# Optimization experiments

Hardware: AMD Instinct MI355X
Metric: run time of the kernel (lower is better)

Reference implementation:

```python
import jax, jax.numpy as jnp
import numpy as np

B, L, DIM, H = 2, 2048, 2048, 16
DH = DIM // H  # 128, size_per_head


def setup_inputs() -> dict:
    key = jax.random.key(0)
    k1, k2, k3, k4, k5, k6 = jax.random.split(key, 6)
    s = 0.02
    return {
        "query_tensor": jax.random.normal(k1, (B, L, DIM), jnp.float32),
        "value_tensor": jax.random.normal(k2, (B, L, DIM), jnp.float32),
        "attention_mask": jax.random.randint(k3, (B, L), 0, 2).astype(jnp.float32),
        "Wq": jax.random.normal(k4, (DIM, DIM), jnp.float32) * s,
        "Wk": jax.random.normal(k5, (DIM, DIM), jnp.float32) * s,
        "Wv": jax.random.normal(k6, (DIM, DIM), jnp.float32) * s,
    }


def reference(query_tensor, value_tensor, attention_mask, Wq, Wk, Wv):
    b, lq, dim = query_tensor.shape
    lv = value_tensor.shape[1]
    # torch Linear: x @ W.T (no bias)
    q = query_tensor @ Wq.T   # [B, Lq, DIM]
    k = value_tensor @ Wk.T   # [B, Lv, DIM]
    v = value_tensor @ Wv.T   # [B, Lv, DIM]
    # split heads -> [B, H, L, DH]
    q = q.reshape(b, lq, H, DH).transpose(0, 2, 1, 3)
    k = k.reshape(b, lv, H, DH).transpose(0, 2, 1, 3)
    v = v.reshape(b, lv, H, DH).transpose(0, 2, 1, 3)
    scores = jnp.einsum('bhqd,bhkd->bhqk', q, k) / jnp.sqrt(jnp.float32(DH))
    # multiplicative per-query mask, broadcast [B,1,Lq,1] -> [B,H,Lq,Lv]
    scores = scores * attention_mask[:, None, :, None]
    probs = jax.nn.softmax(scores, axis=-1)
    attn = jnp.einsum('bhqk,bhkd->bhqd', probs, v)  # [B,H,Lq,DH]
    return attn.transpose(0, 2, 1, 3).reshape(b, lq, dim)
```

## Files before the change

### kernel.cpp

```cpp
#include <hip/hip_runtime.h>
#include <hip/hip_bf16.h>
#include <stdint.h>

#define DIM_ 2048
#define L_   2048
#define B_   2
#define H_   16
#define DH_  128
#define NT_  32

#define QSCALE_ 0.12751743f

typedef __attribute__((ext_vector_type(4))) float fp32x4;
typedef __attribute__((ext_vector_type(8))) short s16x8;

__device__ __forceinline__ unsigned short bf16_rne(float f) {
    unsigned u = __builtin_bit_cast(unsigned, f);
    u += 0x7fffu + ((u >> 16) & 1u);
    return (unsigned short)(u >> 16);
}

__device__ __forceinline__ fp32x4 MFMA(s16x8 a, s16x8 b, fp32x4 c) {
    return __builtin_amdgcn_mfma_f32_16x16x32_bf16(a, b, c, 0, 0, 0);
}

__device__ __forceinline__ void gld16(const void* g, void* l) {
    auto gp = reinterpret_cast<const uint32_t __attribute__((address_space(1)))*>(
        reinterpret_cast<uintptr_t>(g));
    auto lp = reinterpret_cast<uint32_t __attribute__((address_space(3)))*>(
        reinterpret_cast<uintptr_t>(l));
    __builtin_amdgcn_global_load_lds(gp, lp, 16, 0, 0);
}

__device__ __forceinline__ float exp2_raw(float x) {
    float r; asm("v_exp_f32 %0, %1" : "=v"(r) : "v"(x)); return r;
}

__device__ __forceinline__ unsigned cvtpk_bf16(float a, float b) {
    unsigned r; asm("v_cvt_pk_bf16_f32 %0, %1, %2" : "=v"(r) : "v"(a), "v"(b)); return r;
}

__global__ void __launch_bounds__(256)
cvt_all(const float* __restrict__ query, const float* __restrict__ value,
        const float* __restrict__ Wq, const float* __restrict__ Wk,
        const float* __restrict__ Wv,
        unsigned short* __restrict__ qb, unsigned short* __restrict__ vb,
        unsigned short* __restrict__ wqb, unsigned short* __restrict__ wkb,
        unsigned short* __restrict__ wvb)
{
    const int total4 = 7340032;
    int i = blockIdx.x * 256 + threadIdx.x;
    const int stride = gridDim.x * 256;
    for (; i < total4; i += stride) {
        const float4* s; ushort4* d; int off; float sc = 1.0f;
        if (i < 2097152)      { s = (const float4*)query; d = (ushort4*)qb;  off = i; }
        else if (i < 4194304) { s = (const float4*)value; d = (ushort4*)vb;  off = i - 2097152; }
        else if (i < 5242880) { s = (const float4*)Wq;    d = (ushort4*)wqb; off = i - 4194304; sc = QSCALE_; }
        else if (i < 6291456) { s = (const float4*)Wk;    d = (ushort4*)wkb; off = i - 5242880; }
        else                  { s = (const float4*)Wv;    d = (ushort4*)wvb; off = i - 6291456; }
        float4 v = s[off];
        ushort4 o;
        o.x = bf16_rne(v.x * sc); o.y = bf16_rne(v.y * sc);
        o.z = bf16_rne(v.z * sc); o.w = bf16_rne(v.w * sc);
        d[off] = o;
    }
}

__global__ void __launch_bounds__(512, 2)
gemm_qkv8(const unsigned short* __restrict__ qb, const unsigned short* __restrict__ vb,
          const unsigned short* __restrict__ wqb, const unsigned short* __restrict__ wkb,
          const unsigned short* __restrict__ wvb, const float* __restrict__ mask,
          unsigned short* __restrict__ q_ws, unsigned short* __restrict__ k_ws,
          unsigned short* __restrict__ v_ws)
{
    __shared__ __align__(16) char As_[3][32768];
    __shared__ __align__(16) char Bs_[3][16384];

    const int tid  = threadIdx.x;
    const int lane = tid & 63;
    const int wid  = tid >> 6;
    const int wm   = wid >> 1;
    const int wn   = wid & 1;
    const int lr   = lane & 15;
    const int lg   = lane >> 4;

    const int g     = (blockIdx.x & 7) * 96 + (blockIdx.x >> 3);
    const int which = g >> 8;
    const int rb    = g & 255;
    const int bm    = (rb >> 4) << 8;
    const int bn    = (rb & 15) << 7;

    const unsigned short* Xb = (which == 0) ? qb : vb;
    const unsigned short* Wb = (which == 0) ? wqb : (which == 1) ? wkb : wvb;

    const int srow = tid >> 3;
    const int scol = ((tid & 7) ^ (((tid >> 5) & 1) << 1)) * 8;
    const unsigned short* gA = Xb + (size_t)(bm + srow) * DIM_ + scol;
    const unsigned short* gB = Wb + (size_t)(bn + srow) * DIM_ + scol;
    const int ldst = wid * 1024;

    const int xsw  = ((lr >> 2) & 1) << 5;
    const int abase = wm * 8192 + lr * 128 + ((lg * 16) ^ xsw);
    const int bbase = wn * 8192 + lr * 128 + ((lg * 16) ^ xsw);

    fp32x4 acc[4][4] = {};

#define STGH1(BUF, T) do {                                                        \
    gld16(gA + (size_t)(T) * 64,                 &As_[BUF][ldst]);                \
    gld16(gA + (size_t)64 * DIM_ + (T) * 64,     &As_[BUF][8192 + ldst]);         \
    gld16(gB + (size_t)(T) * 64,                 &Bs_[BUF][ldst]);                \
} while (0)
#define STGH2(BUF, T) do {                                                        \
    gld16(gA + (size_t)128 * DIM_ + (T) * 64,    &As_[BUF][16384 + ldst]);        \
    gld16(gA + (size_t)192 * DIM_ + (T) * 64,    &As_[BUF][24576 + ldst]);        \
    gld16(gB + (size_t)64 * DIM_ + (T) * 64,     &Bs_[BUF][8192 + ldst]);         \
} while (0)

#define PH(AB, BB, KK, STG_STMT, WAIT_STMT) do {                                  \
    s16x8 fa0 = *reinterpret_cast<const s16x8*>(&(AB)[abase + (KK)*64]);          \
    s16x8 fa1 = *reinterpret_cast<const s16x8*>(&(AB)[abase + (KK)*64 + 2048]);   \
    s16x8 fa2 = *reinterpret_cast<const s16x8*>(&(AB)[abase + (KK)*64 + 4096]);   \
    s16x8 fa3 = *reinterpret_cast<const s16x8*>(&(AB)[abase + (KK)*64 + 6144]);   \
    s16x8 fb0 = *reinterpret_cast<const s16x8*>(&(BB)[bbase + (KK)*64]);          \
    s16x8 fb1 = *reinterpret_cast<const s16x8*>(&(BB)[bbase + (KK)*64 + 2048]);   \
    s16x8 fb2 = *reinterpret_cast<const s16x8*>(&(BB)[bbase + (KK)*64 + 4096]);   \
    s16x8 fb3 = *reinterpret_cast<const s16x8*>(&(BB)[bbase + (KK)*64 + 6144]);   \
    STG_STMT;                                                                     \
    __builtin_amdgcn_s_barrier();                                                 \
    asm volatile("s_waitcnt lgkmcnt(0)" ::: "memory");                            \
    __builtin_amdgcn_s_setprio(1);                                                \
    acc[0][0] = MFMA(fa0, fb0, acc[0][0]);                                        \
    acc[0][1] = MFMA(fa0, fb1, acc[0][1]);                                        \
    acc[0][2] = MFMA(fa0, fb2, acc[0][2]);                                        \
    acc[0][3] = MFMA(fa0, fb3, acc[0][3]);                                        \
    acc[1][0] = MFMA(fa1, fb0, acc[1][0]);                                        \
    acc[1][1] = MFMA(fa1, fb1, acc[1][1]);                                        \
    acc[1][2] = MFMA(fa1, fb2, acc[1][2]);                                        \
    acc[1][3] = MFMA(fa1, fb3, acc[1][3]);                                        \
    acc[2][0] = MFMA(fa2, fb0, acc[2][0]);                                        \
    acc[2][1] = MFMA(fa2, fb1, acc[2][1]);                                        \
    acc[2][2] = MFMA(fa2, fb2, acc[2][2]);                                        \
    acc[2][3] = MFMA(fa2, fb3, acc[2][3]);                                        \
    acc[3][0] = MFMA(fa3, fb0, acc[3][0]);                                        \
    acc[3][1] = MFMA(fa3, fb1, acc[3][1]);                                        \
    acc[3][2] = MFMA(fa3, fb2, acc[3][2]);                                        \
    acc[3][3] = MFMA(fa3, fb3, acc[3][3]);                                        \
    __builtin_amdgcn_s_setprio(0);                                                \
    WAIT_STMT;                                                                    \
    __builtin_amdgcn_s_barrier();                                                 \
} while (0)

#define W6 asm volatile("s_waitcnt vmcnt(6)" ::: "memory")
#define W0 asm volatile("s_waitcnt vmcnt(0)" ::: "memory")

    STGH1(0, 0); STGH2(0, 0);
    STGH1(1, 1); STGH2(1, 1);
    W6;
    __builtin_amdgcn_s_barrier();

    for (int t = 0; t < NT_ - 2; ++t) {
        char* Ab = &As_[t % 3][0];
        char* Bb = &Bs_[t % 3][0];
        const int bnx = (t + 2) % 3;
        PH(Ab, Bb, 0, STGH1(bnx, t + 2), (void)0);
        PH(Ab, Bb, 1, STGH2(bnx, t + 2), W6);
    }
    {
        char* Ab = &As_[0][0]; char* Bb = &Bs_[0][0];
        PH(Ab, Bb, 0, (void)0, (void)0);
        PH(Ab, Bb, 1, (void)0, W0);
    }
    {
        char* Ab = &As_[1][0]; char* Bb = &Bs_[1][0];
        PH(Ab, Bb, 0, (void)0, (void)0);
        PH(Ab, Bb, 1, (void)0, (void)0);
    }

    const int bb = bm >> 11;
    const size_t bh0 = (size_t)(bb * H_) * (L_ * DH_);
    const int rbase = bm + wm * 64;
    const int cbase = bn + wn * 64;

    if (which == 2) {
        #pragma unroll
        for (int mf = 0; mf < 4; ++mf) {
            int l0 = (rbase + mf * 16 + lg * 4) & (L_ - 1);
            #pragma unroll
            for (int nf = 0; nf < 4; ++nf) {
                int dc = cbase + nf * 16 + lr;
                int h = dc >> 7, d = dc & 127;
                size_t off = bh0 + (size_t)h * (L_ * DH_)
                    + (size_t)(((l0 >> 5) * 8 + (d >> 4)) * 512
                    + ((d & 15) + (((l0 >> 3) & 3) << 4)) * 8 + (l0 & 7));
                ushort4 pk;
                pk.x = bf16_rne(acc[mf][nf][0]);
                pk.y = bf16_rne(acc[mf][nf][1]);
                pk.z = bf16_rne(acc[mf][nf][2]);
                pk.w = bf16_rne(acc[mf][nf][3]);
                *reinterpret_cast<ushort4*>(&v_ws[off]) = pk;
            }
        }
    } else if (which == 1) {
        #pragma unroll
        for (int mf = 0; mf < 4; ++mf)
            #pragma unroll
            for (int rr = 0; rr < 4; ++rr) {
                int l = (rbase + mf * 16 + lg * 4 + rr) & (L_ - 1);
                #pragma unroll
                for (int nf = 0; nf < 4; ++nf) {
                    int dc = cbase + nf * 16 + lr;
                    int h = dc >> 7, d = dc & 127;
                    size_t off = bh0 + (size_t)h * (L_ * DH_)
                        + (size_t)(((l >> 4) * 4 + (d >> 5)) * 512
                        + ((l & 15) + (((d >> 3) & 3) << 4)) * 8 + (d & 7));
                    k_ws[off] = bf16_rne(acc[mf][nf][rr]);
                }
            }
    } else {
        const float* mrow = mask + bb * L_;
        #pragma unroll
        for (int mf = 0; mf < 4; ++mf)
            #pragma unroll
            for (int rr = 0; rr < 4; ++rr) {
                int l = (rbase + mf * 16 + lg * 4 + rr) & (L_ - 1);
                float mvv = mrow[l];
                #pragma unroll
                for (int nf = 0; nf < 4; ++nf) {
                    int dc = cbase + nf * 16 + lr;
                    int h = dc >> 7, d = dc & 127;
                    q_ws[bh0 + (size_t)h * (L_ * DH_) + (size_t)l * DH_ + d]
                        = bf16_rne(acc[mf][nf][rr] * mvv);
                }
            }
    }
#undef STGH1
#undef STGH2
#undef PH
#undef W6
#undef W0
}

__global__ void __launch_bounds__(256, 2)
attn_fused3(const unsigned short* __restrict__ qw, const unsigned short* __restrict__ kfr,
            const unsigned short* __restrict__ vfr, float* __restrict__ out)
{
    __shared__ __align__(16) char Ks[2][16384];
    __shared__ __align__(16) char Pl[4][4608];

    const int tid  = threadIdx.x;
    const int lane = tid & 63;
    const int wid  = tid >> 6;
    const int lr   = lane & 15;
    const int lg   = lane >> 4;

    const int p  = (blockIdx.x & 7) * 64 + (blockIdx.x >> 3);
    const int bh = p >> 4;
    const int qt = p & 15;
    const int b  = bh >> 4;
    const int h  = bh & 15;
    const int q0 = qt * 128 + wid * 32;

    const unsigned short* qbase = qw  + (size_t)bh * (L_ * DH_);
    const unsigned short* kbase = kfr + (size_t)bh * (L_ * DH_);
    const unsigned short* vbase = vfr + (size_t)bh * (L_ * DH_);

    s16x8 qf[2][4];
    #pragma unroll
    for (int qs = 0; qs < 2; ++qs)
        #pragma unroll
        for (int kc = 0; kc < 4; ++kc)
            qf[qs][kc] = *reinterpret_cast<const s16x8*>(
                &qbase[(size_t)(q0 + qs * 16 + lr) * DH_ + kc * 32 + lg * 8]);

    s16x8 ones;
    #pragma unroll
    for (int i = 0; i < 8; ++i) ones[i] = (short)0x3F80;

    fp32x4 acc[2][8] = {};
    fp32x4 racc[2] = {};

    char* P = &Pl[wid][0];

    auto STAGE = [&](int buf, int t) {
        const unsigned short* g = kbase + (size_t)t * 8192;
        #pragma unroll
        for (int c = 0; c < 4; ++c)
            gld16(g + c * 2048 + tid * 8, &Ks[buf][c * 4096 + wid * 1024]);
    };

    STAGE(0, 0);
    __syncthreads();

    for (int t = 0; t < L_ / 64; ++t) {
        const int buf = t & 1;
        if (t + 1 < L_ / 64) STAGE(buf ^ 1, t + 1);

        s16x8 vv0[8], vv1[8];
        #pragma unroll
        for (int ds = 0; ds < 8; ++ds)
            vv0[ds] = *reinterpret_cast<const s16x8*>(
                &vbase[(size_t)t * 8192 + (0 * 8 + ds) * 512 + lane * 8]);

        fp32x4 s2[2][4] = {};
        __builtin_amdgcn_s_setprio(1);
        #pragma unroll
        for (int kvs = 0; kvs < 4; ++kvs)
            #pragma unroll
            for (int kc = 0; kc < 4; ++kc) {
                s16x8 kf = *reinterpret_cast<const s16x8*>(
                    Ks[buf] + (kvs * 4 + kc) * 1024 + lane * 16);
                s2[0][kvs] = MFMA(kf, qf[0][kc], s2[0][kvs]);
                s2[1][kvs] = MFMA(kf, qf[1][kc], s2[1][kvs]);
            }
        __builtin_amdgcn_s_setprio(0);

        #pragma unroll
        for (int qs = 0; qs < 2; ++qs)
            #pragma unroll
            for (int kvs = 0; kvs < 4; ++kvs) {
                float e0 = exp2_raw(s2[qs][kvs][0]);
                float e1 = exp2_raw(s2[qs][kvs][1]);
                float e2 = exp2_raw(s2[qs][kvs][2]);
                float e3 = exp2_raw(s2[qs][kvs][3]);
                uint2 pk;
                pk.x = cvtpk_bf16(e0, e1);
                pk.y = cvtpk_bf16(e2, e3);
                *reinterpret_cast<uint2*>(P + qs * 2304 + lr * 144 + kvs * 32 + lg * 8) = pk;
            }

        #pragma unroll
        for (int ds = 0; ds < 8; ++ds)
            vv1[ds] = *reinterpret_cast<const s16x8*>(
                &vbase[(size_t)t * 8192 + (1 * 8 + ds) * 512 + lane * 8]);

        __builtin_amdgcn_s_setprio(1);
        #pragma unroll
        for (int qs = 0; qs < 2; ++qs) {
            s16x8 pa0 = *reinterpret_cast<const s16x8*>(P + qs * 2304 + lr * 144 + 0 * 64 + lg * 16);
            s16x8 pa1 = *reinterpret_cast<const s16x8*>(P + qs * 2304 + lr * 144 + 1 * 64 + lg * 16);
            racc[qs] = MFMA(pa0, ones, racc[qs]);
            racc[qs] = MFMA(pa1, ones, racc[qs]);
            #pragma unroll
            for (int ds = 0; ds < 8; ++ds) {
                acc[qs][ds] = MFMA(pa0, vv0[ds], acc[qs][ds]);
                acc[qs][ds] = MFMA(pa1, vv1[ds], acc[qs][ds]);
            }
        }
        __builtin_amdgcn_s_setprio(0);

        __syncthreads();
    }

    #pragma unroll
    for (int qs = 0; qs < 2; ++qs) {
        float inv[4];
        #pragma unroll
        for (int r = 0; r < 4; ++r) inv[r] = 1.0f / racc[qs][r];
        #pragma unroll
        for (int ds = 0; ds < 8; ++ds)
            #pragma unroll
            for (int r = 0; r < 4; ++r)
                out[((size_t)(b * L_ + q0 + qs * 16 + lg * 4 + r)) * DIM_ + h * DH_ + ds * 16 + lr]
                    = acc[qs][ds][r] * inv[r];
    }
}

extern "C" void kernel_launch(void* const* d_in, const int* in_sizes, int n_in,
                              void* d_out, int out_size, void* d_ws, size_t ws_size,
                              hipStream_t stream) {
    const float* query = (const float*)d_in[0];
    const float* value = (const float*)d_in[1];
    const float* mask  = (const float*)d_in[2];
    const float* Wq    = (const float*)d_in[3];
    const float* Wk    = (const float*)d_in[4];
    const float* Wv    = (const float*)d_in[5];
    float* out = (float*)d_out;

    const size_t elems  = (size_t)B_ * H_ * L_ * DH_;
    const size_t welems = elems / 2;
    unsigned short* q_ws = (unsigned short*)d_ws;
    unsigned short* k_ws = q_ws + elems;
    unsigned short* v_ws = k_ws + elems;

    unsigned short* qbf  = v_ws + elems;
    unsigned short* vbf  = qbf + elems;
    unsigned short* wqbf = vbf + elems;
    unsigned short* wkbf = wqbf + welems;
    unsigned short* wvbf = wkbf + welems;

    dim3 blk(256, 1, 1);

    cvt_all<<<dim3(2048, 1, 1), blk, 0, stream>>>(query, value, Wq, Wk, Wv,
                                                  qbf, vbf, wqbf, wkbf, wvbf);
    gemm_qkv8<<<dim3(768, 1, 1), dim3(512, 1, 1), 0, stream>>>(
        qbf, vbf, wqbf, wkbf, wvbf, mask, q_ws, k_ws, v_ws);

    attn_fused3<<<dim3(512, 1, 1), blk, 0, stream>>>(q_ws, k_ws, v_ws, out);
}
```

Measured before the change: 214.2 us.

## Restructure projection GEMM main loop to one barrier per K-tile with XOR swizzle

```diff
diff --git a/kernel.cpp b/kernel.cpp
--- a/kernel.cpp
+++ b/kernel.cpp
@@ -94,86 +94,74 @@
     const unsigned short* Wb = (which == 0) ? wqb : (which == 1) ? wkb : wvb;
 
     const int srow = tid >> 3;
-    const int scol = ((tid & 7) ^ (((tid >> 5) & 1) << 1)) * 8;
+    const int scol = ((tid & 7) ^ ((tid >> 3) & 7)) * 8;
     const unsigned short* gA = Xb + (size_t)(bm + srow) * DIM_ + scol;
     const unsigned short* gB = Wb + (size_t)(bn + srow) * DIM_ + scol;
     const int ldst = wid * 1024;
 
-    const int xsw  = ((lr >> 2) & 1) << 5;
-    const int abase = wm * 8192 + lr * 128 + ((lg * 16) ^ xsw);
-    const int bbase = wn * 8192 + lr * 128 + ((lg * 16) ^ xsw);
+    const int r7   = (lr & 7) << 4;
+    const int arow = (wm * 64 + lr) * 128;
+    const int brow = (wn * 64 + lr) * 128;
+    const int off0 = (lg << 4) ^ r7;
+    const int off1 = (64 | (lg << 4)) ^ r7;
 
     fp32x4 acc[4][4] = {};
 
-#define STGH1(BUF, T) do {                                                        \
-    gld16(gA + (size_t)(T) * 64,                 &As_[BUF][ldst]);                \
-    gld16(gA + (size_t)64 * DIM_ + (T) * 64,     &As_[BUF][8192 + ldst]);         \
-    gld16(gB + (size_t)(T) * 64,                 &Bs_[BUF][ldst]);                \
+#define STG6(SA, SB, T) do {                                                      \
+    gld16(gA + (size_t)(T) * 64,                 (SA) + ldst);                    \
+    gld16(gA + (size_t)64  * DIM_ + (T) * 64,    (SA) + 8192  + ldst);            \
+    gld16(gA + (size_t)128 * DIM_ + (T) * 64,    (SA) + 16384 + ldst);            \
+    gld16(gA + (size_t)192 * DIM_ + (T) * 64,    (SA) + 24576 + ldst);            \
+    gld16(gB + (size_t)(T) * 64,                 (SB) + ldst);                    \
+    gld16(gB + (size_t)64  * DIM_ + (T) * 64,    (SB) + 8192  + ldst);            \
 } while (0)
-#define STGH2(BUF, T) do {                                                        \
-    gld16(gA + (size_t)128 * DIM_ + (T) * 64,    &As_[BUF][16384 + ldst]);        \
-    gld16(gA + (size_t)192 * DIM_ + (T) * 64,    &As_[BUF][24576 + ldst]);        \
-    gld16(gB + (size_t)64 * DIM_ + (T) * 64,     &Bs_[BUF][8192 + ldst]);         \
-} while (0)
-
-#define PH(AB, BB, KK, STG_STMT, WAIT_STMT) do {                                  \
-    s16x8 fa0 = *reinterpret_cast<const s16x8*>(&(AB)[abase + (KK)*64]);          \
-    s16x8 fa1 = *reinterpret_cast<const s16x8*>(&(AB)[abase + (KK)*64 + 2048]);   \
-    s16x8 fa2 = *reinterpret_cast<const s16x8*>(&(AB)[abase + (KK)*64 + 4096]);   \
-    s16x8 fa3 = *reinterpret_cast<const s16x8*>(&(AB)[abase + (KK)*64 + 6144]);   \
-    s16x8 fb0 = *reinterpret_cast<const s16x8*>(&(BB)[bbase + (KK)*64]);          \
-    s16x8 fb1 = *reinterpret_cast<const s16x8*>(&(BB)[bbase + (KK)*64 + 2048]);   \
-    s16x8 fb2 = *reinterpret_cast<const s16x8*>(&(BB)[bbase + (KK)*64 + 4096]);   \
-    s16x8 fb3 = *reinterpret_cast<const s16x8*>(&(BB)[bbase + (KK)*64 + 6144]);   \
-    STG_STMT;                                                                     \
-    __builtin_amdgcn_s_barrier();                                                 \
-    asm volatile("s_waitcnt lgkmcnt(0)" ::: "memory");                            \
-    __builtin_amdgcn_s_setprio(1);                                                \
-    acc[0][0] = MFMA(fa0, fb0, acc[0][0]);                                        \
-    acc[0][1] = MFMA(fa0, fb1, acc[0][1]);                                        \
-    acc[0][2] = MFMA(fa0, fb2, acc[0][2]);                                        \
-    acc[0][3] = MFMA(fa0, fb3, acc[0][3]);                                        \
-    acc[1][0] = MFMA(fa1, fb0, acc[1][0]);                                        \
-    acc[1][1] = MFMA(fa1, fb1, acc[1][1]);                                        \
-    acc[1][2] = MFMA(fa1, fb2, acc[1][2]);                                        \
-    acc[1][3] = MFMA(fa1, fb3, acc[1][3]);                                        \
-    acc[2][0] = MFMA(fa2, fb0, acc[2][0]);                                        \
-    acc[2][1] = MFMA(fa2, fb1, acc[2][1]);                                        \
-    acc[2][2] = MFMA(fa2, fb2, acc[2][2]);                                        \
-    acc[2][3] = MFMA(fa2, fb3, acc[2][3]);                                        \
-    acc[3][0] = MFMA(fa3, fb0, acc[3][0]);                                        \
-    acc[3][1] = MFMA(fa3, fb1, acc[3][1]);                                        \
-    acc[3][2] = MFMA(fa3, fb2, acc[3][2]);                                        \
-    acc[3][3] = MFMA(fa3, fb3, acc[3][3]);                                        \
-    __builtin_amdgcn_s_setprio(0);                                                \
-    WAIT_STMT;                                                                    \
-    __builtin_amdgcn_s_barrier();                                                 \
-} while (0)
-
-#define W6 asm volatile("s_waitcnt vmcnt(6)" ::: "memory")
-#define W0 asm volatile("s_waitcnt vmcnt(0)" ::: "memory")
-
-    STGH1(0, 0); STGH2(0, 0);
-    STGH1(1, 1); STGH2(1, 1);
-    W6;
+
+    STG6(&As_[0][0], &Bs_[0][0], 0);
+    STG6(&As_[1][0], &Bs_[1][0], 1);
+    asm volatile("s_waitcnt vmcnt(6)" ::: "memory");
     __builtin_amdgcn_s_barrier();
 
-    for (int t = 0; t < NT_ - 2; ++t) {
+    for (int t = 0; t < NT_; ++t) {
         char* Ab = &As_[t % 3][0];
         char* Bb = &Bs_[t % 3][0];
-        const int bnx = (t + 2) % 3;
-        PH(Ab, Bb, 0, STGH1(bnx, t + 2), (void)0);
-        PH(Ab, Bb, 1, STGH2(bnx, t + 2), W6);
-    }
-    {
-        char* Ab = &As_[0][0]; char* Bb = &Bs_[0][0];
-        PH(Ab, Bb, 0, (void)0, (void)0);
-        PH(Ab, Bb, 1, (void)0, W0);
-    }
-    {
-        char* Ab = &As_[1][0]; char* Bb = &Bs_[1][0];
-        PH(Ab, Bb, 0, (void)0, (void)0);
-        PH(Ab, Bb, 1, (void)0, (void)0);
+        if (t < NT_ - 2) {
+            char* An = &As_[(t + 2) % 3][0];
+            char* Bn = &Bs_[(t + 2) % 3][0];
+            STG6(An, Bn, t + 2);
+        }
+
+        s16x8 fa0[4], fa1[4], fb0[4], fb1[4];
+        #pragma unroll
+        for (int mi = 0; mi < 4; ++mi) {
+            fa0[mi] = *reinterpret_cast<const s16x8*>(&Ab[arow + mi * 2048 + off0]);
+            fa1[mi] = *reinterpret_cast<const s16x8*>(&Ab[arow + mi * 2048 + off1]);
+        }
+        #pragma unroll
+        for (int nf = 0; nf < 4; ++nf) {
+            fb0[nf] = *reinterpret_cast<const s16x8*>(&Bb[brow + nf * 2048 + off0]);
+            fb1[nf] = *reinterpret_cast<const s16x8*>(&Bb[brow + nf * 2048 + off1]);
+        }
+
+        __builtin_amdgcn_s_setprio(1);
+        #pragma unroll
+        for (int mi = 0; mi < 4; ++mi)
+            #pragma unroll
+            for (int nf = 0; nf < 4; ++nf)
+                acc[mi][nf] = MFMA(fa0[mi], fb0[nf], acc[mi][nf]);
+        #pragma unroll
+        for (int mi = 0; mi < 4; ++mi)
+            #pragma unroll
+            for (int nf = 0; nf < 4; ++nf)
+                acc[mi][nf] = MFMA(fa1[mi], fb1[nf], acc[mi][nf]);
+        __builtin_amdgcn_s_setprio(0);
+
+        if (t < NT_ - 2) {
+            asm volatile("s_waitcnt vmcnt(6)" ::: "memory");
+            __builtin_amdgcn_s_barrier();
+        } else if (t == NT_ - 2) {
+            asm volatile("s_waitcnt vmcnt(0)" ::: "memory");
+            __builtin_amdgcn_s_barrier();
+        }
     }
 
     const int bb = bm >> 11;
@@ -233,11 +221,7 @@
                 }
             }
     }
-#undef STGH1
-#undef STGH2
-#undef PH
-#undef W6
-#undef W0
+#undef STG6
 }
 
 __global__ void __launch_bounds__(256, 2)
```

New measurement: 203.3 us. 1.05x faster.
